# Kernel optimization log

Hardware: AMD Instinct MI355X
Metric: run time of the kernel (lower is better)

The kernel has to match this reference:

```python
import jax, jax.numpy as jnp
import numpy as np

N_NODES = 50000
N_EDGES = 800000
D_IN = 64
D_HID = 64
D_OUT = 64


def setup_inputs() -> dict:
    key = jax.random.key(0)
    ks = jax.random.split(key, 10)
    x = jax.random.normal(ks[0], (N_NODES, D_IN), dtype=jnp.float32)
    src = jax.random.randint(ks[1], (N_EDGES,), 0, N_NODES, dtype=jnp.int32)
    dst = jax.random.randint(ks[2], (N_EDGES,), 0, N_NODES, dtype=jnp.int32)
    s = 1.0 / np.sqrt(D_IN)
    W0 = jax.random.uniform(ks[3], (D_IN, D_HID), jnp.float32, -s, s)
    b0 = jnp.zeros((D_HID,), jnp.float32)
    W1 = jax.random.uniform(ks[4], (D_HID, D_HID), jnp.float32, -s, s)
    b1 = jnp.zeros((D_HID,), jnp.float32)
    W2 = jax.random.uniform(ks[5], (D_HID, D_OUT), jnp.float32, -s, s)
    b2 = jnp.zeros((D_OUT,), jnp.float32)
    return {"x": x, "src": src, "dst": dst, "W0": W0, "b0": b0,
            "W1": W1, "b1": b1, "W2": W2, "b2": b2}


def reference(x, src, dst, W0, b0, W1, b1, W2, b2):
    N = x.shape[0]
    # in-degree (constant across layers)
    deg = jax.ops.segment_sum(jnp.ones(src.shape[0], x.dtype), dst, num_segments=N)
    inv = (1.0 / (deg + 1.0))[:, None]  # [N,1] gcn normalizer (deg + self)

    def sage_gcn(h, W, b):
        # gather neighbor feats along edges, scatter-add to destinations
        agg = jax.ops.segment_sum(h[src], dst, num_segments=N)  # [N,d]
        h_neigh = (agg + h) * inv
        return h_neigh @ W + b

    h = sage_gcn(x, W0, b0)
    h = jax.nn.relu(h)
    h = sage_gcn(h, W1, b1)
    h = jax.nn.relu(h)
    h = sage_gcn(h, W2, b2)
    return h
```

## Files before the change

kernel.cpp:

```cpp
#include <hip/hip_runtime.h>

#define D 64

__global__ void count_deg_kernel(const int* __restrict__ dst, int* __restrict__ deg, int nE) {
    int e4 = (blockIdx.x * blockDim.x + threadIdx.x) * 4;
    if (e4 + 3 < nE) {
        int4 d = *(const int4*)(dst + e4);
        atomicAdd(&deg[d.x], 1);
        atomicAdd(&deg[d.y], 1);
        atomicAdd(&deg[d.z], 1);
        atomicAdd(&deg[d.w], 1);
    } else {
        for (int e = e4; e < nE; ++e) atomicAdd(&deg[dst[e]], 1);
    }
}

__global__ __launch_bounds__(256) void scan_a_kernel(const int* __restrict__ deg,
                                                     int* __restrict__ row_ptr,
                                                     int* __restrict__ blocksums, int N) {
    __shared__ int s[256];
    int t = threadIdx.x;
    int i = blockIdx.x * 256 + t;
    int v = (i < N) ? deg[i] : 0;
    s[t] = v;
    __syncthreads();
    #pragma unroll
    for (int d = 1; d < 256; d <<= 1) {
        int u = (t >= d) ? s[t - d] : 0;
        __syncthreads();
        s[t] += u;
        __syncthreads();
    }
    if (i < N) row_ptr[i] = s[t] - v;
    if (t == 255) blocksums[blockIdx.x] = s[255];
}

__global__ __launch_bounds__(256) void scan_b_kernel(int* __restrict__ blocksums,
                                                     int* __restrict__ row_ptr,
                                                     int nb, int N) {
    __shared__ int s[256];
    int t = threadIdx.x;
    int v = (t < nb) ? blocksums[t] : 0;
    s[t] = v;
    __syncthreads();
    #pragma unroll
    for (int d = 1; d < 256; d <<= 1) {
        int u = (t >= d) ? s[t - d] : 0;
        __syncthreads();
        s[t] += u;
        __syncthreads();
    }
    if (t < nb) blocksums[t] = s[t] - v;
    if (t == 255) row_ptr[N] = s[255];
}

__global__ __launch_bounds__(256) void scan_c_kernel(int* __restrict__ row_ptr,
                                                     int* __restrict__ cursor,
                                                     const int* __restrict__ blocksums, int N) {
    int i = blockIdx.x * 256 + threadIdx.x;
    if (i < N) {
        int r = row_ptr[i] + blocksums[blockIdx.x];
        row_ptr[i] = r;
        cursor[i] = r;
    }
}

__global__ __launch_bounds__(256) void fill_csr_sliced_kernel(
    const int* __restrict__ src, const int* __restrict__ dst,
    int* __restrict__ cursor, int* __restrict__ col,
    int nE, int slice_size)
{
    const int g  = blockIdx.x & 7;
    const int gb = blockIdx.x >> 3;
    const int lo = g * slice_size;
    const int hi = lo + slice_size;
    int e4 = (gb * 256 + (int)threadIdx.x) * 4;
    if (e4 + 3 < nE) {
        int4 d = *(const int4*)(dst + e4);
        bool m0 = (d.x >= lo) & (d.x < hi);
        bool m1 = (d.y >= lo) & (d.y < hi);
        bool m2 = (d.z >= lo) & (d.z < hi);
        bool m3 = (d.w >= lo) & (d.w < hi);
        if (m0 | m1 | m2 | m3) {
            int4 s = *(const int4*)(src + e4);
            if (m0) col[atomicAdd(&cursor[d.x], 1)] = s.x;
            if (m1) col[atomicAdd(&cursor[d.y], 1)] = s.y;
            if (m2) col[atomicAdd(&cursor[d.z], 1)] = s.z;
            if (m3) col[atomicAdd(&cursor[d.w], 1)] = s.w;
        }
    } else if (e4 < nE) {
        for (int e = e4; e < nE; ++e) {
            int dd = dst[e];
            if (dd >= lo && dd < hi) col[atomicAdd(&cursor[dd], 1)] = src[e];
        }
    }
}

__global__ __launch_bounds__(256, 4) void sage_layer_kernel(
    const float* __restrict__ h, const int* __restrict__ row_ptr,
    const int* __restrict__ col, const float* __restrict__ W,
    const float* __restrict__ bias, float* __restrict__ out,
    int N, int do_relu)
{
    __shared__ float Wlds[D * D];
    {
        const float4* W4 = (const float4*)W;
        float4* Wl4 = (float4*)Wlds;
        #pragma unroll
        for (int t = 0; t < 4; ++t)
            Wl4[t * 256 + threadIdx.x] = W4[t * 256 + threadIdx.x];
    }
    __syncthreads();

    const int lane = threadIdx.x & 63;
    const int sub  = lane >> 4;
    const int fq   = lane & 15;
    const int w    = threadIdx.x >> 6;
    const float bj = bias[lane];

    const float4* __restrict__ h4 = (const float4*)h;

    const int nwaves = gridDim.x * 4;
    for (int i0 = blockIdx.x * 4 + w; i0 < N; i0 += nwaves) {
        const int i   = __builtin_amdgcn_readfirstlane(i0);
        const int rs  = __builtin_amdgcn_readfirstlane(row_ptr[i]);
        const int re  = __builtin_amdgcn_readfirstlane(row_ptr[i + 1]);
        const int deg = re - rs;

        float4 a0 = {0,0,0,0}, a1 = {0,0,0,0}, a2 = {0,0,0,0}, a3 = {0,0,0,0};
        int last_iv = 0;

        for (int e0 = rs; e0 < re; e0 += 64) {
            int ee = e0 + lane;
            int idxv = col[(ee < re) ? ee : (re - 1)];
            last_iv = idxv;
            int rem = re - e0;
            int steps = (((rem < 64) ? rem : 64) + 3) >> 2;
            int t = 0;
            for (; t + 4 <= steps; t += 4) {
                int base = (t << 2) + sub;
                int s0 = __shfl(idxv, base);
                int s1 = __shfl(idxv, base + 4);
                int s2 = __shfl(idxv, base + 8);
                int s3 = __shfl(idxv, base + 12);
                float4 v0 = h4[(size_t)s0 * 16 + fq];
                float4 v1 = h4[(size_t)s1 * 16 + fq];
                float4 v2 = h4[(size_t)s2 * 16 + fq];
                float4 v3 = h4[(size_t)s3 * 16 + fq];
                a0.x += v0.x; a0.y += v0.y; a0.z += v0.z; a0.w += v0.w;
                a1.x += v1.x; a1.y += v1.y; a1.z += v1.z; a1.w += v1.w;
                a2.x += v2.x; a2.y += v2.y; a2.z += v2.z; a2.w += v2.w;
                a3.x += v3.x; a3.y += v3.y; a3.z += v3.z; a3.w += v3.w;
            }
            for (; t < steps; ++t) {
                int s0 = __shfl(idxv, (t << 2) + sub);
                float4 v0 = h4[(size_t)s0 * 16 + fq];
                a0.x += v0.x; a0.y += v0.y; a0.z += v0.z; a0.w += v0.w;
            }
        }

        float4 tt;
        tt.x = (a0.x + a1.x) + (a2.x + a3.x);
        tt.y = (a0.y + a1.y) + (a2.y + a3.y);
        tt.z = (a0.z + a1.z) + (a2.z + a3.z);
        tt.w = (a0.w + a1.w) + (a2.w + a3.w);
        tt.x += __shfl_xor(tt.x, 16); tt.x += __shfl_xor(tt.x, 32);
        tt.y += __shfl_xor(tt.y, 16); tt.y += __shfl_xor(tt.y, 32);
        tt.z += __shfl_xor(tt.z, 16); tt.z += __shfl_xor(tt.z, 32);
        tt.w += __shfl_xor(tt.w, 16); tt.w += __shfl_xor(tt.w, 32);

        int pad = (-deg) & 3;
        if (deg > 0 && pad) {
            int last = __shfl(last_iv, 63);
            float4 vl = h4[(size_t)last * 16 + fq];
            float fp = (float)pad;
            tt.x = fmaf(-fp, vl.x, tt.x);
            tt.y = fmaf(-fp, vl.y, tt.y);
            tt.z = fmaf(-fp, vl.z, tt.z);
            tt.w = fmaf(-fp, vl.w, tt.w);
        }

        float4 hs = h4[(size_t)i * 16 + fq];
        float invd = 1.0f / (float)(deg + 1);
        tt.x = (tt.x + hs.x) * invd;
        tt.y = (tt.y + hs.y) * invd;
        tt.z = (tt.z + hs.z) * invd;
        tt.w = (tt.w + hs.w) * invd;

        float o0 = bj, o1 = 0.0f, o2 = 0.0f, o3 = 0.0f;
        #pragma unroll
        for (int k = 0; k < D; k += 4) {
            const int q = k >> 2;
            int t0 = __builtin_amdgcn_readlane(__float_as_int(tt.x), q);
            int t1 = __builtin_amdgcn_readlane(__float_as_int(tt.y), q);
            int t2 = __builtin_amdgcn_readlane(__float_as_int(tt.z), q);
            int t3 = __builtin_amdgcn_readlane(__float_as_int(tt.w), q);
            o0 = fmaf(__int_as_float(t0), Wlds[(k + 0) * D + lane], o0);
            o1 = fmaf(__int_as_float(t1), Wlds[(k + 1) * D + lane], o1);
            o2 = fmaf(__int_as_float(t2), Wlds[(k + 2) * D + lane], o2);
            o3 = fmaf(__int_as_float(t3), Wlds[(k + 3) * D + lane], o3);
        }
        float o = (o0 + o1) + (o2 + o3);
        if (do_relu) o = fmaxf(o, 0.0f);
        out[(size_t)i * D + lane] = o;
    }
}

extern "C" void kernel_launch(void* const* d_in, const int* in_sizes, int n_in,
                              void* d_out, int out_size, void* d_ws, size_t ws_size,
                              hipStream_t stream) {
    const float* x   = (const float*)d_in[0];
    const int*   src = (const int*)d_in[1];
    const int*   dst = (const int*)d_in[2];
    const float* W0  = (const float*)d_in[3];
    const float* b0  = (const float*)d_in[4];
    const float* W1  = (const float*)d_in[5];
    const float* b1  = (const float*)d_in[6];
    const float* W2  = (const float*)d_in[7];
    const float* b2  = (const float*)d_in[8];
    float* out = (float*)d_out;

    const int N = in_sizes[0] / D;
    const int E = in_sizes[1];

    const int scan_blocks = (N + 255) / 256;

    char* ws = (char*)d_ws;
    size_t off = 0;
    auto alloc = [&](size_t bytes) -> void* {
        void* p = ws + off;
        off = (off + bytes + 255) & ~(size_t)255;
        return p;
    };
    int*   deg       = (int*)  alloc((size_t)N * sizeof(int));
    int*   row_ptr   = (int*)  alloc((size_t)(N + 1) * sizeof(int));
    int*   cursor    = (int*)  alloc((size_t)N * sizeof(int));
    int*   blocksums = (int*)  alloc((size_t)scan_blocks * sizeof(int));
    int*   col       = (int*)  alloc((size_t)E * sizeof(int));
    float* h1        = (float*)alloc((size_t)N * D * sizeof(float));
    float* h2        = (float*)alloc((size_t)N * D * sizeof(float));

    hipMemsetAsync(deg, 0, (size_t)N * sizeof(int), stream);
    const int e4_blocks = (E / 4 + 255) / 256;
    count_deg_kernel<<<e4_blocks, 256, 0, stream>>>(dst, deg, E);
    scan_a_kernel<<<scan_blocks, 256, 0, stream>>>(deg, row_ptr, blocksums, N);
    scan_b_kernel<<<1, 256, 0, stream>>>(blocksums, row_ptr, scan_blocks, N);
    scan_c_kernel<<<scan_blocks, 256, 0, stream>>>(row_ptr, cursor, blocksums, N);
    const int slice_size = (N + 7) / 8;
    fill_csr_sliced_kernel<<<e4_blocks * 8, 256, 0, stream>>>(src, dst, cursor, col, E, slice_size);

    const int layer_blocks = 4096;

    sage_layer_kernel<<<layer_blocks, 256, 0, stream>>>(x,  row_ptr, col, W0, b0, h1,  N, 1);
    sage_layer_kernel<<<layer_blocks, 256, 0, stream>>>(h1, row_ptr, col, W1, b1, h2,  N, 1);
    sage_layer_kernel<<<layer_blocks, 256, 0, stream>>>(h2, row_ptr, col, W2, b2, out, N, 0);
}
```

Measured before the change: 286.0 us.

## Partition neighbor gathers into source slabs with per-block rotated slab order

The neighbor gather loop now buckets each 64-edge chunk by source-node slab (eight slices), compacts the indices with ballot/mbcnt/ds_permute, and processes one slab at a time. Each block starts at a different slab, so concurrently running waves tend to touch different regions of the feature matrix, which is meant to improve cache/TLB locality of the random gathers. The padding-correction trick is replaced by explicit masking, and the self-feature load is hoisted earlier. In exchange it adds eight ballot passes per chunk, extra permutes and shuffles, and less memory-level parallelism, since only two loads are in flight per step instead of four.

```diff
diff --git a/kernel.cpp b/kernel.cpp
--- a/kernel.cpp
+++ b/kernel.cpp
@@ -100,7 +100,7 @@
     const float* __restrict__ h, const int* __restrict__ row_ptr,
     const int* __restrict__ col, const float* __restrict__ W,
     const float* __restrict__ bias, float* __restrict__ out,
-    int N, int do_relu)
+    int N, int do_relu, int slice)
 {
     __shared__ float Wlds[D * D];
     {
@@ -117,6 +117,7 @@
     const int fq   = lane & 15;
     const int w    = threadIdx.x >> 6;
     const float bj = bias[lane];
+    const int slab0 = blockIdx.x & 7;
 
     const float4* __restrict__ h4 = (const float4*)h;
 
@@ -127,60 +128,58 @@
         const int re  = __builtin_amdgcn_readfirstlane(row_ptr[i + 1]);
         const int deg = re - rs;
 
-        float4 a0 = {0,0,0,0}, a1 = {0,0,0,0}, a2 = {0,0,0,0}, a3 = {0,0,0,0};
-        int last_iv = 0;
+        float4 hs = h4[(size_t)i * 16 + fq];
+
+        float4 a0 = {0,0,0,0}, a1 = {0,0,0,0};
 
         for (int e0 = rs; e0 < re; e0 += 64) {
             int ee = e0 + lane;
             int idxv = col[(ee < re) ? ee : (re - 1)];
-            last_iv = idxv;
             int rem = re - e0;
-            int steps = (((rem < 64) ? rem : 64) + 3) >> 2;
-            int t = 0;
-            for (; t + 4 <= steps; t += 4) {
-                int base = (t << 2) + sub;
-                int s0 = __shfl(idxv, base);
-                int s1 = __shfl(idxv, base + 4);
-                int s2 = __shfl(idxv, base + 8);
-                int s3 = __shfl(idxv, base + 12);
-                float4 v0 = h4[(size_t)s0 * 16 + fq];
-                float4 v1 = h4[(size_t)s1 * 16 + fq];
-                float4 v2 = h4[(size_t)s2 * 16 + fq];
-                float4 v3 = h4[(size_t)s3 * 16 + fq];
-                a0.x += v0.x; a0.y += v0.y; a0.z += v0.z; a0.w += v0.w;
-                a1.x += v1.x; a1.y += v1.y; a1.z += v1.z; a1.w += v1.w;
-                a2.x += v2.x; a2.y += v2.y; a2.z += v2.z; a2.w += v2.w;
-                a3.x += v3.x; a3.y += v3.y; a3.z += v3.z; a3.w += v3.w;
+            int nvalid = (rem < 64) ? rem : 64;
+            bool lane_ok = lane < nvalid;
+
+            for (int p = 0; p < 8; ++p) {
+                const int sl = (slab0 + p) & 7;
+                const int lo = sl * slice;
+                bool in_slab = lane_ok && ((unsigned)(idxv - lo) < (unsigned)slice);
+                unsigned long long mask = __ballot(in_slab);
+                int cnt = __popcll(mask);
+                if (cnt == 0) continue;
+                int pos = __builtin_amdgcn_mbcnt_hi((unsigned)(mask >> 32),
+                          __builtin_amdgcn_mbcnt_lo((unsigned)mask, 0));
+                int dslot = in_slab ? pos : (cnt + lane - pos);
+                int cidx = __builtin_amdgcn_ds_permute(dslot << 2, idxv);
+
+                for (int t0 = 0; t0 < cnt; t0 += 8) {
+                    int sl0 = t0 + sub;
+                    int q0 = __shfl(cidx, (sl0 < cnt) ? sl0 : 0);
+                    float4 v0 = h4[(size_t)q0 * 16 + fq];
+                    if (t0 + 4 < cnt) {
+                        int sl1 = t0 + 4 + sub;
+                        int q1 = __shfl(cidx, (sl1 < cnt) ? sl1 : 0);
+                        float4 v1 = h4[(size_t)q1 * 16 + fq];
+                        if (sl1 < cnt) {
+                            a1.x += v1.x; a1.y += v1.y; a1.z += v1.z; a1.w += v1.w;
+                        }
+                    }
+                    if (sl0 < cnt) {
+                        a0.x += v0.x; a0.y += v0.y; a0.z += v0.z; a0.w += v0.w;
+                    }
+                }
             }
-            for (; t < steps; ++t) {
-                int s0 = __shfl(idxv, (t << 2) + sub);
-                float4 v0 = h4[(size_t)s0 * 16 + fq];
-                a0.x += v0.x; a0.y += v0.y; a0.z += v0.z; a0.w += v0.w;
-            }
         }
 
         float4 tt;
-        tt.x = (a0.x + a1.x) + (a2.x + a3.x);
-        tt.y = (a0.y + a1.y) + (a2.y + a3.y);
-        tt.z = (a0.z + a1.z) + (a2.z + a3.z);
-        tt.w = (a0.w + a1.w) + (a2.w + a3.w);
+        tt.x = a0.x + a1.x;
+        tt.y = a0.y + a1.y;
+        tt.z = a0.z + a1.z;
+        tt.w = a0.w + a1.w;
         tt.x += __shfl_xor(tt.x, 16); tt.x += __shfl_xor(tt.x, 32);
         tt.y += __shfl_xor(tt.y, 16); tt.y += __shfl_xor(tt.y, 32);
         tt.z += __shfl_xor(tt.z, 16); tt.z += __shfl_xor(tt.z, 32);
         tt.w += __shfl_xor(tt.w, 16); tt.w += __shfl_xor(tt.w, 32);
 
-        int pad = (-deg) & 3;
-        if (deg > 0 && pad) {
-            int last = __shfl(last_iv, 63);
-            float4 vl = h4[(size_t)last * 16 + fq];
-            float fp = (float)pad;
-            tt.x = fmaf(-fp, vl.x, tt.x);
-            tt.y = fmaf(-fp, vl.y, tt.y);
-            tt.z = fmaf(-fp, vl.z, tt.z);
-            tt.w = fmaf(-fp, vl.w, tt.w);
-        }
-
-        float4 hs = h4[(size_t)i * 16 + fq];
         float invd = 1.0f / (float)(deg + 1);
         tt.x = (tt.x + hs.x) * invd;
         tt.y = (tt.y + hs.y) * invd;
@@ -251,7 +250,7 @@
 
     const int layer_blocks = 4096;
 
-    sage_layer_kernel<<<layer_blocks, 256, 0, stream>>>(x,  row_ptr, col, W0, b0, h1,  N, 1);
-    sage_layer_kernel<<<layer_blocks, 256, 0, stream>>>(h1, row_ptr, col, W1, b1, h2,  N, 1);
-    sage_layer_kernel<<<layer_blocks, 256, 0, stream>>>(h2, row_ptr, col, W2, b2, out, N, 0);
-}
+    sage_layer_kernel<<<layer_blocks, 256, 0, stream>>>(x,  row_ptr, col, W0, b0, h1,  N, 1, slice_size);
+    sage_layer_kernel<<<layer_blocks, 256, 0, stream>>>(h1, row_ptr, col, W1, b1, h2,  N, 1, slice_size);
+    sage_layer_kernel<<<layer_blocks, 256, 0, stream>>>(h2, row_ptr, col, W2, b2, out, N, 0, slice_size);
+}
```

Measured after the change: 365.6 us. 1.28x slower.
